# Kernel optimization log

Measured on AMD Instinct MI355X. Metric: run time of the kernel, lower is better.

## Reference

```python
import jax, jax.numpy as jnp
import numpy as np

D_MODEL = 1024
DFF = 4096
SPARSITY = 0.5
EPS = 1e-6


def layer_norm(x, gamma, beta):
    mu = jnp.mean(x, axis=-1, keepdims=True)
    var = jnp.mean(jnp.square(x - mu), axis=-1, keepdims=True)
    return (x - mu) * jax.lax.rsqrt(var + EPS) * gamma + beta


def setup_inputs() -> dict:
    key = jax.random.key(0)
    ks = jax.random.split(key, 8)
    B, S, d, f = 4, 2048, D_MODEL, DFF
    s = 1.0 / np.sqrt(d)
    return {
        "x": jax.random.normal(ks[0], (B, S, d), dtype=jnp.float32),
        "Wq": jax.random.normal(ks[1], (d, d), dtype=jnp.float32) * s,
        "bq": jnp.zeros((d,), jnp.float32),
        "Wk": jax.random.normal(ks[2], (d, d), dtype=jnp.float32) * s,
        "bk": jnp.zeros((d,), jnp.float32),
        "Wv": jax.random.normal(ks[3], (d, d), dtype=jnp.float32) * s,
        "bv": jnp.zeros((d,), jnp.float32),
        "W1": jax.random.normal(ks[4], (d, f), dtype=jnp.float32) * s,
        "b1": jnp.zeros((f,), jnp.float32),
        "W2": jax.random.normal(ks[5], (f, d), dtype=jnp.float32) * (1.0 / np.sqrt(f)),
        "b2": jnp.zeros((d,), jnp.float32),
        "gamma1": jnp.ones((d,), jnp.float32),
        "beta1": jnp.zeros((d,), jnp.float32),
        "gamma2": jnp.ones((d,), jnp.float32),
        "beta2": jnp.zeros((d,), jnp.float32),
    }


def reference(x, Wq, bq, Wk, bk, Wv, bv, W1, b1, W2, b2, gamma1, beta1, gamma2, beta2):
    B, S, d = x.shape
    q = x @ Wq + bq
    k = x @ Wk + bk
    v = x @ Wv + bv
    # scores: [B, S, S], scaled by sqrt(d_model)
    scores = jnp.einsum("bqd,bkd->bqk", q, k) / jnp.sqrt(jnp.float32(d))
    # top-k sparsification: keep scores >= row-wise k-th largest, else 0
    topk = int(SPARSITY * S)
    top_vals = jax.lax.top_k(scores, topk)[0]  # sorted descending
    threshold = top_vals[..., -1:]
    sparse_scores = jnp.where(scores >= threshold, scores, jnp.zeros_like(scores))
    attn = jax.nn.softmax(sparse_scores, axis=-1)
    attn_out = jnp.einsum("bqk,bkd->bqd", attn, v)
    out1 = layer_norm(x + attn_out, gamma1, beta1)
    ffn = jax.nn.relu(out1 @ W1 + b1) @ W2 + b2
    return layer_norm(out1 + ffn, gamma2, beta2)
```

## Files before the change

### kernel.cpp

```cpp
#include <hip/hip_runtime.h>
#include <cstdint>

typedef unsigned short u16;
typedef __attribute__((ext_vector_type(8))) short s16x8;
typedef __attribute__((ext_vector_type(4))) unsigned short u16x4;
typedef __attribute__((ext_vector_type(4))) float f32x4;

__device__ __forceinline__ u16 f2bf(float f) {
  union { float f; uint32_t u; } c; c.f = f;
  uint32_t r = c.u + 0x7FFFu + ((c.u >> 16) & 1u);
  return (u16)(r >> 16);
}
__device__ __forceinline__ float bf2f(u16 b) {
  union { uint32_t u; float f; } c; c.u = ((uint32_t)b) << 16;
  return c.f;
}
__device__ __forceinline__ float wave_sum_f(float v) {
#pragma unroll
  for (int o = 32; o > 0; o >>= 1) v += __shfl_xor(v, o);
  return v;
}
__device__ __forceinline__ float wave_max_f(float v) {
#pragma unroll
  for (int o = 32; o > 0; o >>= 1) v = fmaxf(v, __shfl_xor(v, o));
  return v;
}
__device__ __forceinline__ void gload16(const u16* g, u16* l) {
  __builtin_amdgcn_global_load_lds(
      (const __attribute__((address_space(1))) unsigned int*)g,
      (__attribute__((address_space(3))) unsigned int*)l,
      16, 0, 0);
}

__global__ __launch_bounds__(256)
void cast_f32_bf16(const float* __restrict__ in, u16* __restrict__ out) {
  long i = ((long)blockIdx.x * 256 + threadIdx.x) * 4;
  f32x4 v = *(const f32x4*)(in + i);
  u16x4 o;
#pragma unroll
  for (int j = 0; j < 4; ++j) o[j] = f2bf(v[j]);
  *(u16x4*)(out + i) = o;
}

__global__ __launch_bounds__(256)
void concat3(const float* __restrict__ a, const float* __restrict__ b,
             const float* __restrict__ c, float* __restrict__ o) {
  int i = blockIdx.x * 256 + threadIdx.x;
  o[i] = i < 1024 ? a[i] : (i < 2048 ? b[i - 1024] : c[i - 2048]);
}

__global__ __launch_bounds__(256)
void transpose_cast_f32_bf16(const float* __restrict__ in, u16* __restrict__ out,
                             int R, int C) {
  __shared__ float tile[32][33];
  int r0 = blockIdx.y * 32, c0 = blockIdx.x * 32;
  int tid = threadIdx.x;
  int tr = tid >> 3, tc4 = (tid & 7) * 4;
  f32x4 v = *(const f32x4*)(in + (long)(r0 + tr) * C + c0 + tc4);
#pragma unroll
  for (int j = 0; j < 4; ++j) tile[tr][tc4 + j] = v[j];
  __syncthreads();
  u16x4 o;
#pragma unroll
  for (int j = 0; j < 4; ++j) o[j] = f2bf(tile[tc4 + j][tr]);
  *(u16x4*)(out + (long)(c0 + tr) * R + r0 + tc4) = o;
}

__global__ __launch_bounds__(256)
void transpose_bf16(const u16* __restrict__ in, u16* __restrict__ out,
                    int R, int C, int in_rs, long in_batch, long out_batch) {
  __shared__ u16 tile[32][36];
  const long zin = (long)blockIdx.z * in_batch;
  const long zout = (long)blockIdx.z * out_batch;
  int r0 = blockIdx.y * 32, c0 = blockIdx.x * 32;
  int tid = threadIdx.x;
  int tr = tid >> 3, tc4 = (tid & 7) * 4;
  u16x4 v = *(const u16x4*)(in + zin + (long)(r0 + tr) * in_rs + c0 + tc4);
#pragma unroll
  for (int j = 0; j < 4; ++j) tile[tr][tc4 + j] = v[j];
  __syncthreads();
  u16x4 o;
#pragma unroll
  for (int j = 0; j < 4; ++j) o[j] = tile[tc4 + j][tr];
  *(u16x4*)(out + zout + (long)(c0 + tr) * R + r0 + tc4) = o;
}

#define TBM 256
#define TBK 64

enum { EPI_BF16_BIAS = 0, EPI_BF16_SCALE = 1, EPI_BF16 = 2,
       EPI_RELU_BF16_BIAS = 3, EPI_F32_BIAS_RESIDBF = 4 };

#define QUAD(MFA)                                                             \
  _Pragma("unroll")                                                           \
  for (int mf = (MFA); mf < (MFA) + 2; ++mf)                                  \
    _Pragma("unroll")                                                         \
    for (int nf = 0; nf < 4; ++nf) {                                          \
      acc[mf][nf] = __builtin_amdgcn_mfma_f32_16x16x32_bf16(                  \
          af[mf][0], bfr[nf][0], acc[mf][nf], 0, 0, 0);                       \
      acc[mf][nf] = __builtin_amdgcn_mfma_f32_16x16x32_bf16(                  \
          af[mf][1], bfr[nf][1], acc[mf][nf], 0, 0, 0);                       \
    }

template <int BN_, int EPI>
__global__ __launch_bounds__(512, 2)
void gemm8p(const u16* __restrict__ A, const u16* __restrict__ Bt,
            const float* __restrict__ bias, const u16* __restrict__ resid,
            void* __restrict__ Cout, int M, int N, int K, int lda, int ldb,
            int tx, int ty, long long batchA, long long batchB, long long batchC,
            float scale) {
  constexpr int MF = (BN_ == 256) ? 8 : 4;
  constexpr int NBI = BN_ / 128;
  __shared__ u16 As[2][TBM * TBK];
  __shared__ u16 Bs[2][BN_ * TBK];

  const int nwg = gridDim.x;
  const int orig = blockIdx.x;
  const int q = nwg >> 3, r = nwg & 7;
  const int xcd = orig & 7, idx = orig >> 3;
  const int wg = (xcd < r ? xcd * (q + 1) : r * (q + 1) + (xcd - r) * q) + idx;
  const int bx = wg % tx;
  const int tmp = wg / tx;
  const int by = tmp % ty;
  const int b  = tmp / ty;

  const u16* Ab = A + (long)b * batchA;
  const u16* Bb = Bt + (long)b * batchB;
  const int row0 = by * TBM;
  const int col0 = bx * BN_;
  const int tid = threadIdx.x;
  const int lane = tid & 63, wid = tid >> 6;
  const int wm = (BN_ == 256) ? (wid >> 2) : (wid >> 1);
  const int wn = (BN_ == 256) ? (wid & 3) : (wid & 1);
  const int rowW = (BN_ == 256) ? wm * 128 : wm * 64;
  const int l15 = lane & 15, g = lane >> 4;

  const int sr = lane >> 3;
  const int sc = ((lane & 7) ^ sr) * 8;
  const int wrow = wid * 8 + sr;

  const int c0 = ((0 + g) ^ (l15 & 7)) * 8;
  const int c1 = ((4 + g) ^ (l15 & 7)) * 8;

  auto stageA = [&](int h, int kt, int bf_) {
#pragma unroll
    for (int j = 0; j < 2; ++j)
      gload16(Ab + (size_t)(row0 + h * 128 + j * 64 + wrow) * lda + kt * TBK + sc,
              &As[bf_][(h * 128 + j * 64 + wid * 8) * TBK]);
  };
  auto stageB = [&](int h, int kt, int bf_) {
#pragma unroll
    for (int j = 0; j < NBI; ++j)
      gload16(Bb + (size_t)(col0 + h * (BN_ / 2) + j * 64 + wrow) * ldb + kt * TBK + sc,
              &Bs[bf_][(h * (BN_ / 2) + j * 64 + wid * 8) * TBK]);
  };

  s16x8 af[MF][2];
  s16x8 bfr[4][2];
  f32x4 acc[MF][4] = {};
  const int nt = K / TBK;

  stageA(0, 0, 0); stageA(1, 0, 0);
  stageB(0, 0, 0); stageB(1, 0, 0);
  if (nt > 1) {
    stageA(0, 1, 1); stageA(1, 1, 1);
    asm volatile("s_waitcnt vmcnt(4)" ::: "memory");
  } else {
    asm volatile("s_waitcnt vmcnt(0)" ::: "memory");
  }
  __builtin_amdgcn_s_barrier();

  for (int t = 0; t < nt; ++t) {
    const int cur = t & 1;
    const u16* Asc = &As[cur][0];
    const u16* Bsc = &Bs[cur][0];

    if constexpr (BN_ == 256) {
#pragma unroll
      for (int nf = 0; nf < 4; ++nf) {
        const int rb = (wn * 64 + nf * 16 + l15) * TBK;
        bfr[nf][0] = *(const s16x8*)(Bsc + rb + c0);
        bfr[nf][1] = *(const s16x8*)(Bsc + rb + c1);
      }
#pragma unroll
      for (int mf = 0; mf < 4; ++mf) {
        const int rb = (rowW + mf * 16 + l15) * TBK;
        af[mf][0] = *(const s16x8*)(Asc + rb + c0);
        af[mf][1] = *(const s16x8*)(Asc + rb + c1);
      }
      if (t + 1 < nt) stageB(0, t + 1, cur ^ 1);
      __builtin_amdgcn_s_barrier();
      __builtin_amdgcn_s_setprio(1);
      QUAD(0)
      __builtin_amdgcn_s_setprio(0);
      __builtin_amdgcn_s_barrier();

#pragma unroll
      for (int mf = 4; mf < 8; ++mf) {
        const int rb = (rowW + mf * 16 + l15) * TBK;
        af[mf][0] = *(const s16x8*)(Asc + rb + c0);
        af[mf][1] = *(const s16x8*)(Asc + rb + c1);
      }
      if (t + 1 < nt) stageB(1, t + 1, cur ^ 1);
      __builtin_amdgcn_s_barrier();
      __builtin_amdgcn_s_setprio(1);
      QUAD(2)
      __builtin_amdgcn_s_setprio(0);
      asm volatile("s_waitcnt lgkmcnt(0)" ::: "memory");
      __builtin_amdgcn_sched_barrier(0);
      __builtin_amdgcn_s_barrier();

      if (t + 2 < nt) stageA(0, t + 2, cur);
      __builtin_amdgcn_s_barrier();
      __builtin_amdgcn_s_setprio(1);
      QUAD(4)
      __builtin_amdgcn_s_setprio(0);
      __builtin_amdgcn_s_barrier();

      if (t + 2 < nt) stageA(1, t + 2, cur);
      __builtin_amdgcn_s_barrier();
      __builtin_amdgcn_s_setprio(1);
      QUAD(6)
      __builtin_amdgcn_s_setprio(0);
      if (t + 1 < nt) {
        if (t + 2 < nt) asm volatile("s_waitcnt vmcnt(4)" ::: "memory");
        else            asm volatile("s_waitcnt vmcnt(0)" ::: "memory");
      }
      __builtin_amdgcn_s_barrier();
    } else {
#pragma unroll
      for (int nf = 0; nf < 4; ++nf) {
        const int rb = (wn * 64 + nf * 16 + l15) * TBK;
        bfr[nf][0] = *(const s16x8*)(Bsc + rb + c0);
        bfr[nf][1] = *(const s16x8*)(Bsc + rb + c1);
      }
#pragma unroll
      for (int mf = 0; mf < 4; ++mf) {
        const int rb = (rowW + mf * 16 + l15) * TBK;
        af[mf][0] = *(const s16x8*)(Asc + rb + c0);
        af[mf][1] = *(const s16x8*)(Asc + rb + c1);
      }
      if (t + 1 < nt) { stageB(0, t + 1, cur ^ 1); stageB(1, t + 1, cur ^ 1); }
      asm volatile("s_waitcnt lgkmcnt(0)" ::: "memory");
      __builtin_amdgcn_sched_barrier(0);
      __builtin_amdgcn_s_barrier();
      __builtin_amdgcn_s_setprio(1);
      QUAD(0)
      __builtin_amdgcn_s_setprio(0);
      if (t + 2 < nt) { stageA(0, t + 2, cur); stageA(1, t + 2, cur); }
      __builtin_amdgcn_s_setprio(1);
      QUAD(2)
      __builtin_amdgcn_s_setprio(0);
      if (t + 1 < nt) {
        if (t + 2 < nt) asm volatile("s_waitcnt vmcnt(4)" ::: "memory");
        else            asm volatile("s_waitcnt vmcnt(0)" ::: "memory");
        __builtin_amdgcn_s_barrier();
      }
    }
  }

  const long cb = (long)b * batchC;
#pragma unroll
  for (int mf = 0; mf < MF; ++mf) {
    const int rbase = row0 + rowW + mf * 16 + g * 4;
#pragma unroll
    for (int nf = 0; nf < 4; ++nf) {
      const int col = col0 + wn * 64 + nf * 16 + l15;
#pragma unroll
      for (int rr = 0; rr < 4; ++rr) {
        const long cidx = cb + (long)(rbase + rr) * N + col;
        float v = acc[mf][nf][rr];
        if (EPI == EPI_BF16_BIAS) {
          ((u16*)Cout)[cidx] = f2bf(v + bias[col]);
        } else if (EPI == EPI_BF16_SCALE) {
          ((u16*)Cout)[cidx] = f2bf(v * scale);
        } else if (EPI == EPI_BF16) {
          ((u16*)Cout)[cidx] = f2bf(v);
        } else if (EPI == EPI_RELU_BF16_BIAS) {
          ((u16*)Cout)[cidx] = f2bf(fmaxf(v + bias[col], 0.0f));
        } else {
          ((float*)Cout)[cidx] = v + bias[col] + bf2f(resid[cidx]);
        }
      }
    }
  }
}

__global__ __launch_bounds__(256)
void topk_softmax(const u16* __restrict__ scores, u16* __restrict__ P, int topk) {
  const int lane = threadIdx.x & 63, wid = threadIdx.x >> 6;
  const long row = (long)blockIdx.x * 4 + wid;
  const long rowoff = row * 2048;

  float v[32]; uint32_t kv[32];
  const uint32_t* src = (const uint32_t*)(scores + rowoff);
#pragma unroll
  for (int j = 0; j < 16; ++j) {
    uint32_t w = src[j * 64 + lane];
    v[2 * j]     = bf2f((u16)(w & 0xFFFFu));
    v[2 * j + 1] = bf2f((u16)(w >> 16));
  }
#pragma unroll
  for (int j = 0; j < 32; ++j) {
    union { float f; uint32_t u; } c; c.f = v[j];
    kv[j] = (c.u & 0x80000000u) ? ~c.u : (c.u | 0x80000000u);
  }
  float m = v[0];
#pragma unroll
  for (int j = 1; j < 32; ++j) m = fmaxf(m, v[j]);
  m = wave_max_f(m);

  uint32_t cur = 0;
  for (int bit = 31; bit >= 0; --bit) {
    const uint32_t cand = cur | (1u << bit);
    int c = 0;
#pragma unroll
    for (int j = 0; j < 32; ++j)
      c += (int)__popcll(__ballot(kv[j] >= cand));
    if (c >= topk) cur = cand;
  }

  const float mm = fmaxf(m, 0.0f);
  float p[32], s = 0.0f;
#pragma unroll
  for (int j = 0; j < 32; ++j) {
    float val = (kv[j] >= cur) ? v[j] : 0.0f;
    p[j] = __expf(val - mm);
    s += p[j];
  }
  s = wave_sum_f(s);
  const float inv = 1.0f / s;
  uint32_t* dst = (uint32_t*)(P + rowoff);
#pragma unroll
  for (int j = 0; j < 16; ++j) {
    uint32_t w = (uint32_t)f2bf(p[2 * j] * inv) |
                 ((uint32_t)f2bf(p[2 * j + 1] * inv) << 16);
    dst[j * 64 + lane] = w;
  }
}

__global__ __launch_bounds__(256)
void add_ln(const float* __restrict__ a, const u16* __restrict__ r,
            const float* __restrict__ gamma, const float* __restrict__ beta,
            float* __restrict__ outf, u16* __restrict__ outb) {
  const long off = (long)blockIdx.x * 1024;
  const int tid = threadIdx.x, lane = tid & 63, wid = tid >> 6;
  const int c4 = tid * 4;
  __shared__ float sred[4];
  float x[4];
  f32x4 av = *(const f32x4*)(a + off + c4);
  if (r) {
    u16x4 rv = *(const u16x4*)(r + off + c4);
#pragma unroll
    for (int j = 0; j < 4; ++j) x[j] = av[j] + bf2f(rv[j]);
  } else {
#pragma unroll
    for (int j = 0; j < 4; ++j) x[j] = av[j];
  }
  float s = x[0] + x[1] + x[2] + x[3];
  s = wave_sum_f(s);
  if (lane == 0) sred[wid] = s;
  __syncthreads();
  float mu = (sred[0] + sred[1] + sred[2] + sred[3]) * (1.0f / 1024.0f);
  __syncthreads();
  float qv = 0.0f;
#pragma unroll
  for (int j = 0; j < 4; ++j) { float d = x[j] - mu; qv += d * d; }
  qv = wave_sum_f(qv);
  if (lane == 0) sred[wid] = qv;
  __syncthreads();
  float var = (sred[0] + sred[1] + sred[2] + sred[3]) * (1.0f / 1024.0f);
  float inv = rsqrtf(var + 1e-6f);
  f32x4 gv = *(const f32x4*)(gamma + c4);
  f32x4 bv = *(const f32x4*)(beta + c4);
  f32x4 ov; u16x4 ob;
#pragma unroll
  for (int j = 0; j < 4; ++j) {
    float o = (x[j] - mu) * inv * gv[j] + bv[j];
    ov[j] = o; ob[j] = f2bf(o);
  }
  if (outf) *(f32x4*)(outf + off + c4) = ov;
  if (outb) *(u16x4*)(outb + off + c4) = ob;
}

extern "C" void kernel_launch(void* const* d_in, const int* in_sizes, int n_in,
                              void* d_out, int out_size, void* d_ws, size_t ws_size,
                              hipStream_t stream) {
  const float* x   = (const float*)d_in[0];
  const float* Wq  = (const float*)d_in[1];
  const float* bq  = (const float*)d_in[2];
  const float* Wk  = (const float*)d_in[3];
  const float* bk  = (const float*)d_in[4];
  const float* Wv  = (const float*)d_in[5];
  const float* bv  = (const float*)d_in[6];
  const float* W1  = (const float*)d_in[7];
  const float* b1  = (const float*)d_in[8];
  const float* W2  = (const float*)d_in[9];
  const float* b2  = (const float*)d_in[10];
  const float* g1  = (const float*)d_in[11];
  const float* be1 = (const float*)d_in[12];
  const float* g2  = (const float*)d_in[13];
  const float* be2 = (const float*)d_in[14];

  const int Bz = 4, S = 2048, Dm = 1024, Ff = 4096;
  const int M = Bz * S;
  const int N3 = 3 * Dm;

  char* ws = (char*)d_ws;
  const size_t MBy = 1024u * 1024u;
  u16*  wqkvT  = (u16*)(ws + 0 * MBy);
  u16*  w1T    = (u16*)(ws + 6 * MBy);
  u16*  w2T    = (u16*)(ws + 14 * MBy);
  u16*  xbf    = (u16*)(ws + 23 * MBy);
  u16*  qkv    = (u16*)(ws + 39 * MBy);
  u16*  vT     = (u16*)(ws + 87 * MBy);
  float* bqkv  = (float*)(ws + 103 * MBy);
  u16*  scores = (u16*)(ws + 103 * MBy);
  u16*  P      = (u16*)(ws + 167 * MBy);
  u16*  attn   = (u16*)(ws + 135 * MBy);
  u16*  out1b  = (u16*)(ws + 23 * MBy);
  u16*  hbf    = (u16*)(ws + 39 * MBy);
  float* y     = (float*)(ws + 167 * MBy);

  dim3 blk(256);
  dim3 blk8(512);

  cast_f32_bf16<<<dim3((unsigned)((long)M * Dm / 1024)), blk, 0, stream>>>(x, xbf);
  transpose_cast_f32_bf16<<<dim3(Dm / 32, Dm / 32), blk, 0, stream>>>(Wq, wqkvT, Dm, Dm);
  transpose_cast_f32_bf16<<<dim3(Dm / 32, Dm / 32), blk, 0, stream>>>(Wk, wqkvT + 1024 * 1024, Dm, Dm);
  transpose_cast_f32_bf16<<<dim3(Dm / 32, Dm / 32), blk, 0, stream>>>(Wv, wqkvT + 2048 * 1024, Dm, Dm);
  transpose_cast_f32_bf16<<<dim3(Ff / 32, Dm / 32), blk, 0, stream>>>(W1, w1T, Dm, Ff);
  transpose_cast_f32_bf16<<<dim3(Dm / 32, Ff / 32), blk, 0, stream>>>(W2, w2T, Ff, Dm);
  concat3<<<dim3(12), blk, 0, stream>>>(bq, bk, bv, bqkv);

  gemm8p<128, EPI_BF16_BIAS><<<dim3(24 * 32), blk8, 0, stream>>>(
      xbf, wqkvT, bqkv, nullptr, qkv, M, N3, Dm, Dm, Dm, 24, 32, 0, 0, 0, 1.0f);

  transpose_bf16<<<dim3(Dm / 32, S / 32, Bz), blk, 0, stream>>>(
      qkv + 2048, vT, S, Dm, N3, (long)S * N3, (long)Dm * S);

  gemm8p<256, EPI_BF16_SCALE><<<dim3(8 * 8 * Bz), blk8, 0, stream>>>(
      qkv, qkv + 1024, nullptr, nullptr, scores, S, S, Dm, N3, N3, 8, 8,
      (long long)S * N3, (long long)S * N3, (long long)S * S, 0.03125f);

  topk_softmax<<<dim3(Bz * S / 4), blk, 0, stream>>>(scores, P, S / 2);

  gemm8p<128, EPI_BF16><<<dim3(8 * 8 * Bz), blk8, 0, stream>>>(
      P, vT, nullptr, nullptr, attn, S, Dm, S, S, S, 8, 8,
      (long long)S * S, (long long)Dm * S, (long long)S * Dm, 1.0f);

  add_ln<<<dim3(M), blk, 0, stream>>>(x, attn, g1, be1, nullptr, out1b);

  gemm8p<256, EPI_RELU_BF16_BIAS><<<dim3(16 * 32), blk8, 0, stream>>>(
      out1b, w1T, b1, nullptr, hbf, M, Ff, Dm, Dm, Dm, 16, 32, 0, 0, 0, 1.0f);

  gemm8p<128, EPI_F32_BIAS_RESIDBF><<<dim3(8 * 32), blk8, 0, stream>>>(
      hbf, w2T, b2, out1b, y, M, Dm, Ff, Ff, Ff, 8, 32, 0, 0, 0, 1.0f);

  add_ln<<<dim3(M), blk, 0, stream>>>(y, nullptr, g2, be2, (float*)d_out, nullptr);
}
```

Baseline: 383.9 us.

## Triple-buffer A tiles and split BN=128 GEMM loop into four MFMA phases

For the BN=128 GEMM variant, the A tile in shared memory goes from double to triple buffering, so A for step t+2 can be staged into a third buffer. The main loop becomes four phases: each phase loads one A fragment from LDS, issues one global-to-LDS staging load, then runs one MFMA row group between barriers. The aim is to interleave loads with MFMA work more finely and hide latency better. In exchange it uses more LDS, which can limit occupancy, and adds barriers per iteration.

After: 421.2 us. +9.7%, slower.

```diff
diff --git a/kernel.cpp b/kernel.cpp
--- a/kernel.cpp
+++ b/kernel.cpp
@@ -102,6 +102,15 @@
           af[mf][1], bfr[nf][1], acc[mf][nf], 0, 0, 0);                       \
     }
 
+#define MPH(MF_)                                                              \
+  _Pragma("unroll")                                                           \
+  for (int nf = 0; nf < 4; ++nf) {                                            \
+    acc[MF_][nf] = __builtin_amdgcn_mfma_f32_16x16x32_bf16(                   \
+        af[MF_][0], bfr[nf][0], acc[MF_][nf], 0, 0, 0);                       \
+    acc[MF_][nf] = __builtin_amdgcn_mfma_f32_16x16x32_bf16(                   \
+        af[MF_][1], bfr[nf][1], acc[MF_][nf], 0, 0, 0);                       \
+  }
+
 template <int BN_, int EPI>
 __global__ __launch_bounds__(512, 2)
 void gemm8p(const u16* __restrict__ A, const u16* __restrict__ Bt,
@@ -111,7 +120,8 @@
             float scale) {
   constexpr int MF = (BN_ == 256) ? 8 : 4;
   constexpr int NBI = BN_ / 128;
-  __shared__ u16 As[2][TBM * TBK];
+  constexpr int NAB = (BN_ == 128) ? 3 : 2;
+  __shared__ u16 As[NAB][TBM * TBK];
   __shared__ u16 Bs[2][BN_ * TBK];
 
   const int nwg = gridDim.x;
@@ -171,11 +181,10 @@
   __builtin_amdgcn_s_barrier();
 
   for (int t = 0; t < nt; ++t) {
-    const int cur = t & 1;
-    const u16* Asc = &As[cur][0];
-    const u16* Bsc = &Bs[cur][0];
-
     if constexpr (BN_ == 256) {
+      const int cur = t & 1;
+      const u16* Asc = &As[cur][0];
+      const u16* Bsc = &Bs[cur][0];
 #pragma unroll
       for (int nf = 0; nf < 4; ++nf) {
         const int rb = (wn * 64 + nf * 16 + l15) * TBK;
@@ -228,34 +237,69 @@
       }
       __builtin_amdgcn_s_barrier();
     } else {
+      const int a_cur = t % 3;
+      const int a_st  = (t + 2) % 3;
+      const int b_cur = t & 1;
+      const u16* Asc = &As[a_cur][0];
+      const u16* Bsc = &Bs[b_cur][0];
+
 #pragma unroll
       for (int nf = 0; nf < 4; ++nf) {
         const int rb = (wn * 64 + nf * 16 + l15) * TBK;
         bfr[nf][0] = *(const s16x8*)(Bsc + rb + c0);
         bfr[nf][1] = *(const s16x8*)(Bsc + rb + c1);
       }
-#pragma unroll
-      for (int mf = 0; mf < 4; ++mf) {
-        const int rb = (rowW + mf * 16 + l15) * TBK;
-        af[mf][0] = *(const s16x8*)(Asc + rb + c0);
-        af[mf][1] = *(const s16x8*)(Asc + rb + c1);
-      }
-      if (t + 1 < nt) { stageB(0, t + 1, cur ^ 1); stageB(1, t + 1, cur ^ 1); }
-      asm volatile("s_waitcnt lgkmcnt(0)" ::: "memory");
-      __builtin_amdgcn_sched_barrier(0);
-      __builtin_amdgcn_s_barrier();
-      __builtin_amdgcn_s_setprio(1);
-      QUAD(0)
-      __builtin_amdgcn_s_setprio(0);
-      if (t + 2 < nt) { stageA(0, t + 2, cur); stageA(1, t + 2, cur); }
-      __builtin_amdgcn_s_setprio(1);
-      QUAD(2)
-      __builtin_amdgcn_s_setprio(0);
+      {
+        const int rb = (rowW + l15) * TBK;
+        af[0][0] = *(const s16x8*)(Asc + rb + c0);
+        af[0][1] = *(const s16x8*)(Asc + rb + c1);
+      }
+      if (t + 1 < nt) stageB(0, t + 1, b_cur ^ 1);
+      __builtin_amdgcn_s_barrier();
+      __builtin_amdgcn_s_setprio(1);
+      MPH(0)
+      __builtin_amdgcn_s_setprio(0);
+      __builtin_amdgcn_s_barrier();
+
+      {
+        const int rb = (rowW + 16 + l15) * TBK;
+        af[1][0] = *(const s16x8*)(Asc + rb + c0);
+        af[1][1] = *(const s16x8*)(Asc + rb + c1);
+      }
+      if (t + 1 < nt) stageB(1, t + 1, b_cur ^ 1);
+      __builtin_amdgcn_s_barrier();
+      __builtin_amdgcn_s_setprio(1);
+      MPH(1)
+      __builtin_amdgcn_s_setprio(0);
+      __builtin_amdgcn_s_barrier();
+
+      {
+        const int rb = (rowW + 32 + l15) * TBK;
+        af[2][0] = *(const s16x8*)(Asc + rb + c0);
+        af[2][1] = *(const s16x8*)(Asc + rb + c1);
+      }
+      if (t + 2 < nt) stageA(0, t + 2, a_st);
+      __builtin_amdgcn_s_barrier();
+      __builtin_amdgcn_s_setprio(1);
+      MPH(2)
+      __builtin_amdgcn_s_setprio(0);
+      __builtin_amdgcn_s_barrier();
+
+      {
+        const int rb = (rowW + 48 + l15) * TBK;
+        af[3][0] = *(const s16x8*)(Asc + rb + c0);
+        af[3][1] = *(const s16x8*)(Asc + rb + c1);
+      }
+      if (t + 2 < nt) stageA(1, t + 2, a_st);
       if (t + 1 < nt) {
         if (t + 2 < nt) asm volatile("s_waitcnt vmcnt(4)" ::: "memory");
         else            asm volatile("s_waitcnt vmcnt(0)" ::: "memory");
-        __builtin_amdgcn_s_barrier();
-      }
+      }
+      __builtin_amdgcn_s_barrier();
+      __builtin_amdgcn_s_setprio(1);
+      MPH(3)
+      __builtin_amdgcn_s_setprio(0);
+      if (t + 1 < nt) __builtin_amdgcn_s_barrier();
     }
   }
 
```
